# Performance work log

Hardware: AMD Instinct MI355X
Metric: run time of the kernel (lower is better)

The kernel has to match this reference:

```python
import jax, jax.numpy as jnp
import numpy as np

B, T, C, H = 8, 2048, 768, 64  # batch, seq_len, embedding_dim, head_size


def setup_inputs() -> dict:
    key = jax.random.key(0)
    k1, k2, k3, k4 = jax.random.split(key, 4)
    x = jax.random.normal(k1, (B, T, C), dtype=jnp.float32)
    attention_mask = jnp.ones((B, T), dtype=jnp.float32)
    # nn.Linear(C, H, bias=False) weights stored pre-transposed as (C, H)
    scale = 0.02
    Wq = jax.random.normal(k2, (C, H), dtype=jnp.float32) * scale
    Wk = jax.random.normal(k3, (C, H), dtype=jnp.float32) * scale
    Wv = jax.random.normal(k4, (C, H), dtype=jnp.float32) * scale
    return {"x": x, "attention_mask": attention_mask, "Wq": Wq, "Wk": Wk, "Wv": Wv}


def reference(x, attention_mask, Wq, Wk, Wv):
    # x: [B,T,C]; attention_mask: [B,T] (multiplied per query row)
    head_size = Wq.shape[-1]
    q = x @ Wq  # [B,T,H]
    k = x @ Wk  # [B,T,H]
    v = x @ Wv  # [B,T,H]
    inv_sqrt_h = jnp.asarray(1.0 / np.sqrt(head_size), x.dtype)
    s = jnp.einsum('bqh,bkh->bqk', q, k) * inv_sqrt_h  # [B,T,T]
    # attention_mask.unsqueeze(2) * qK ; masked_fill(qK == 0, -inf)
    s = attention_mask[:, :, None] * s
    s = jnp.where(s == 0, -jnp.inf, s)
    # causal tril mask
    seq = x.shape[1]
    tril = jnp.tril(jnp.ones((seq, seq), dtype=bool))
    s = jnp.where(tril[None, :, :], s, -jnp.inf)
    p = jax.nn.softmax(s, axis=-1)
    # dropout p=0.0 -> identity; nan cleanup (fully-masked rows)
    p = jnp.where(jnp.isnan(p), jnp.asarray(0.0, p.dtype), p)
    out = jnp.einsum('bqk,bkh->bqh', p, v)  # [B,T,H]
    return out
```

## Files before the change

### kernel.cpp

```cpp
#include <hip/hip_runtime.h>
#include <hip/hip_bf16.h>

#define B_ 8
#define T_ 2048
#define C_ 768
#define H_ 64
#define BT_ (B_*T_)

typedef __attribute__((ext_vector_type(8))) short bf16x8;
typedef __attribute__((ext_vector_type(4))) float f32x4;

__device__ __forceinline__ unsigned short f2bf(float x) {
    __hip_bfloat16 h = __float2bfloat16(x);
    return __builtin_bit_cast(unsigned short, h);
}

__device__ __forceinline__ bf16x8 cvt8(float4 a, float4 b) {
    bf16x8 r;
    r[0] = (short)f2bf(a.x); r[1] = (short)f2bf(a.y);
    r[2] = (short)f2bf(a.z); r[3] = (short)f2bf(a.w);
    r[4] = (short)f2bf(b.x); r[5] = (short)f2bf(b.y);
    r[6] = (short)f2bf(b.z); r[7] = (short)f2bf(b.w);
    return r;
}

__global__ __launch_bounds__(256) void wprep(
    const float* __restrict__ Wq, const float* __restrict__ Wk,
    const float* __restrict__ Wv, unsigned short* __restrict__ WTf)
{
    const int gc = blockIdx.x;
    const int t  = threadIdx.x;
    const int lane = t >> 2;
    const int j0   = (t & 3) * 2;
    const int q16  = lane & 15, quad = lane >> 4;
    const int k    = gc * 32 + quad * 8 + j0;
    #pragma unroll
    for (int f = 0; f < 12; f++) {
        const int row = f * 16 + q16;
        const int m = row >> 6, n = row & 63;
        const float* __restrict__ W = (m == 0) ? Wq : (m == 1) ? Wk : Wv;
        ushort2 u;
        u.x = f2bf(W[(size_t)k * H_ + n]);
        u.y = f2bf(W[(size_t)(k + 1) * H_ + n]);
        *(ushort2*)(WTf + (((size_t)gc * 12 + f) * 64 + lane) * 8 + j0) = u;
    }
}

__global__ __launch_bounds__(256, 4) void qkv_kernel(
    const float* __restrict__ x, const unsigned short* __restrict__ WTf,
    unsigned short* __restrict__ qF, unsigned short* __restrict__ kF,
    unsigned short* __restrict__ vF)
{
    __shared__ float mrg[3][64][49];
    const int tid  = threadIdx.x;
    const int w    = tid >> 6;
    const int lane = tid & 63;
    const int q16  = lane & 15, quad = lane >> 4;
    const int rowBase = blockIdx.x << 4;
    const int row  = rowBase + q16;

    const float* __restrict__ xp = x + (size_t)row * C_ + w * 192 + quad * 8;

    f32x4 acc[12] = {};
    #pragma unroll
    for (int c = 0; c < 6; c++) {
        const int gc = w * 6 + c;
        const unsigned short* __restrict__ wpc = WTf + ((size_t)gc * 12) * 512 + lane * 8;
        float4 xa = *(const float4*)(xp + c * 32);
        float4 xb = *(const float4*)(xp + c * 32 + 4);
        bf16x8 wf[12];
        #pragma unroll
        for (int f = 0; f < 12; f++)
            wf[f] = *(const bf16x8*)(wpc + f * 512);
        bf16x8 xf = cvt8(xa, xb);
        #pragma unroll
        for (int f = 0; f < 12; f++)
            acc[f] = __builtin_amdgcn_mfma_f32_16x16x32_bf16(wf[f], xf, acc[f], 0, 0, 0);
    }

    if (w > 0) {
        #pragma unroll
        for (int f = 0; f < 12; f++)
            #pragma unroll
            for (int r = 0; r < 4; r++) mrg[w - 1][lane][f * 4 + r] = acc[f][r];
    }
    __syncthreads();
    if (w == 0) {
        #pragma unroll
        for (int j = 0; j < 3; j++)
            #pragma unroll
            for (int f = 0; f < 12; f++)
                #pragma unroll
                for (int r = 0; r < 4; r++) acc[f][r] += mrg[j][lane][f * 4 + r];

        const size_t gt = (size_t)(rowBase >> 4);
        #pragma unroll
        for (int f = 0; f < 8; f++) {
            ushort4 u;
            u.x = f2bf(acc[f][0]); u.y = f2bf(acc[f][1]);
            u.z = f2bf(acc[f][2]); u.w = f2bf(acc[f][3]);
            const int n4 = f & 3;
            const int qp = (2 * n4 + (quad >> 1)) & 3;
            const int j0 = (quad & 1) * 4;
            unsigned short* __restrict__ dst = (f < 4) ? qF : kF;
            *(ushort4*)(dst + ((gt * 2 + (n4 >> 1)) * 64 + q16 + 16 * qp) * 8 + j0) = u;
        }
        const size_t g32 = (size_t)(rowBase >> 5);
        const int qv = ((rowBase >> 4) & 1) * 2 + (q16 >> 3);
        const int jv = q16 & 7;
        #pragma unroll
        for (int f = 8; f < 12; f++)
            #pragma unroll
            for (int r = 0; r < 4; r++)
                vF[((g32 * 4 + (f - 8)) * 64 + quad * 4 + r + 16 * qv) * 8 + jv] =
                    f2bf(acc[f][r]);
    }
}

__global__ __launch_bounds__(256) void attn_kernel(
    const unsigned short* __restrict__ qF, const unsigned short* __restrict__ kF,
    const unsigned short* __restrict__ vF, const float* __restrict__ mask,
    float* __restrict__ out)
{
    __shared__ __align__(16) unsigned short pS[4][16][88];
    __shared__ float oS[3][64][17];
    __shared__ float mlS[3][64][2];

    const int tid  = threadIdx.x;
    const int w    = tid >> 6;
    const int lane = tid & 63;
    const int q16  = lane & 15;
    const int quad = lane >> 4;
    const int bid  = blockIdx.x;
    const int b    = bid & 7;
    const int qt   = 127 - (bid >> 3);
    const int qrow = (qt << 4) + q16;

    const size_t qbase = ((size_t)(b * 128 + qt) * 2) * 512 + lane * 8;
    bf16x8 qf0 = *(const bf16x8*)(qF + qbase);
    bf16x8 qf1 = *(const bf16x8*)(qF + qbase + 512);
    const float maskv = mask[b * T_ + qrow] * 0.125f * 1.44269504f;

    f32x4 o[4] = {};
    float m_run = -__builtin_inff();
    float l_run = 0.f;

    const int niter = ((qt << 4) + 16 + 63) >> 6;
    for (int kt = w; kt < niter; kt += 4) {
        const int kbase = kt << 6;

        bf16x8 kf[8], vf[8];
        #pragma unroll
        for (int sub = 0; sub < 4; sub++) {
            const unsigned short* kp = kF + ((size_t)(b * 128 + kt * 4 + sub) * 2) * 512 + lane * 8;
            kf[2 * sub]     = *(const bf16x8*)(kp);
            kf[2 * sub + 1] = *(const bf16x8*)(kp + 512);
        }
        #pragma unroll
        for (int ht = 0; ht < 4; ht++) {
            const unsigned short* vp = vF + ((size_t)(b * 64 + kt * 2) * 4 + ht) * 512 + lane * 8;
            vf[2 * ht]     = *(const bf16x8*)(vp);
            vf[2 * ht + 1] = *(const bf16x8*)(vp + 4 * 512);
        }

        f32x4 sa[4] = {};
        #pragma unroll
        for (int sub = 0; sub < 4; sub++) {
            sa[sub] = __builtin_amdgcn_mfma_f32_16x16x32_bf16(kf[2 * sub],     qf0, sa[sub], 0, 0, 0);
            sa[sub] = __builtin_amdgcn_mfma_f32_16x16x32_bf16(kf[2 * sub + 1], qf1, sa[sub], 0, 0, 0);
        }

        float s[16];
        #pragma unroll
        for (int sub = 0; sub < 4; sub++)
            #pragma unroll
            for (int r = 0; r < 4; r++) {
                int kidx = kbase + sub * 16 + quad * 4 + r;
                float sv = sa[sub][r] * maskv;
                sv = (sv == 0.f) ? -__builtin_inff() : sv;
                sv = (kidx > qrow) ? -__builtin_inff() : sv;
                s[sub * 4 + r] = sv;
            }

        float mx = s[0];
        #pragma unroll
        for (int i2 = 1; i2 < 16; i2++) mx = fmaxf(mx, s[i2]);
        mx = fmaxf(mx, __shfl_xor(mx, 16));
        mx = fmaxf(mx, __shfl_xor(mx, 32));
        float m_new = fmaxf(m_run, mx);
        float m_use = (m_new == -__builtin_inff()) ? 0.f : m_new;
        float alpha = exp2f(m_run - m_use);
        float p[16], psum = 0.f;
        #pragma unroll
        for (int i2 = 0; i2 < 16; i2++) { p[i2] = exp2f(s[i2] - m_use); psum += p[i2]; }
        psum += __shfl_xor(psum, 16);
        psum += __shfl_xor(psum, 32);
        l_run = l_run * alpha + psum;
        m_run = m_new;
        #pragma unroll
        for (int ht = 0; ht < 4; ht++)
            #pragma unroll
            for (int r = 0; r < 4; r++) o[ht][r] *= alpha;

        #pragma unroll
        for (int sub = 0; sub < 4; sub++) {
            unsigned int lo = (unsigned int)f2bf(p[sub * 4 + 0]) | ((unsigned int)f2bf(p[sub * 4 + 1]) << 16);
            unsigned int hi = (unsigned int)f2bf(p[sub * 4 + 2]) | ((unsigned int)f2bf(p[sub * 4 + 3]) << 16);
            *(uint2*)&pS[w][q16][sub * 16 + quad * 4] = make_uint2(lo, hi);
        }
        bf16x8 pf0 = *(const bf16x8*)&pS[w][q16][quad * 8];
        bf16x8 pf1 = *(const bf16x8*)&pS[w][q16][32 + quad * 8];

        #pragma unroll
        for (int ht = 0; ht < 4; ht++) {
            o[ht] = __builtin_amdgcn_mfma_f32_16x16x32_bf16(vf[2 * ht],     pf0, o[ht], 0, 0, 0);
            o[ht] = __builtin_amdgcn_mfma_f32_16x16x32_bf16(vf[2 * ht + 1], pf1, o[ht], 0, 0, 0);
        }
    }

    if (w > 0) {
        mlS[w - 1][lane][0] = m_run;
        mlS[w - 1][lane][1] = l_run;
        #pragma unroll
        for (int ht = 0; ht < 4; ht++)
            #pragma unroll
            for (int r = 0; r < 4; r++) oS[w - 1][lane][ht * 4 + r] = o[ht][r];
    }
    __syncthreads();
    if (w == 0) {
        float mm[3], ll[3];
        float m = m_run;
        #pragma unroll
        for (int j = 0; j < 3; j++) {
            mm[j] = mlS[j][lane][0]; ll[j] = mlS[j][lane][1];
            m = fmaxf(m, mm[j]);
        }
        float mu = (m == -__builtin_inff()) ? 0.f : m;
        float a0 = exp2f(m_run - mu);
        float aj[3];
        float l = l_run * a0;
        #pragma unroll
        for (int j = 0; j < 3; j++) { aj[j] = exp2f(mm[j] - mu); l += ll[j] * aj[j]; }
        float invl = (l > 0.f) ? (1.f / l) : 0.f;
        #pragma unroll
        for (int ht = 0; ht < 4; ht++) {
            float4 ov;
            float vx = o[ht][0] * a0, vy = o[ht][1] * a0, vz = o[ht][2] * a0, vw2 = o[ht][3] * a0;
            #pragma unroll
            for (int j = 0; j < 3; j++) {
                vx += oS[j][lane][ht * 4 + 0] * aj[j];
                vy += oS[j][lane][ht * 4 + 1] * aj[j];
                vz += oS[j][lane][ht * 4 + 2] * aj[j];
                vw2 += oS[j][lane][ht * 4 + 3] * aj[j];
            }
            ov.x = vx * invl; ov.y = vy * invl; ov.z = vz * invl; ov.w = vw2 * invl;
            *(float4*)(out + ((size_t)(b * T_) + qrow) * H_ + ht * 16 + quad * 4) = ov;
        }
    }
}

extern "C" void kernel_launch(void* const* d_in, const int* in_sizes, int n_in,
                              void* d_out, int out_size, void* d_ws, size_t ws_size,
                              hipStream_t stream) {
    const float* x    = (const float*)d_in[0];
    const float* mask = (const float*)d_in[1];
    const float* Wq   = (const float*)d_in[2];
    const float* Wk   = (const float*)d_in[3];
    const float* Wv   = (const float*)d_in[4];
    float* out = (float*)d_out;

    unsigned short* qf = (unsigned short*)d_ws;
    unsigned short* kf = qf + (size_t)BT_ * H_;
    unsigned short* vf = kf + (size_t)BT_ * H_;
    unsigned short* wt = vf + (size_t)BT_ * H_;

    wprep<<<24, 256, 0, stream>>>(Wq, Wk, Wv, wt);
    qkv_kernel<<<BT_ / 16, 256, 0, stream>>>(x, wt, qf, kf, vf);
    attn_kernel<<<B_ * (T_ / 16), 256, 0, stream>>>(qf, kf, vf, mask, out);
}
```

Before: 122.7 us.

## Process 32 rows per QKV block to reuse weight fragments; coalesce weight prep via LDS

The QKV projection kernel now handles two 16-row tiles per block, so each loaded bf16 weight fragment feeds two MFMAs. This halves the weight traffic per row and the number of blocks. The weight-prep kernel is rewritten to read rows coalesced into a shared tile and transpose them there, and it is spread over 72 blocks instead of 24. The cost is more accumulator registers, reflected in lowering the occupancy hint to 2, plus an extra LDS merge phase with added barriers.

```diff
diff --git a/kernel.cpp b/kernel.cpp
--- a/kernel.cpp
+++ b/kernel.cpp
@@ -28,25 +28,37 @@
     const float* __restrict__ Wq, const float* __restrict__ Wk,
     const float* __restrict__ Wv, unsigned short* __restrict__ WTf)
 {
-    const int gc = blockIdx.x;
-    const int t  = threadIdx.x;
-    const int lane = t >> 2;
-    const int j0   = (t & 3) * 2;
-    const int q16  = lane & 15, quad = lane >> 4;
-    const int k    = gc * 32 + quad * 8 + j0;
-    #pragma unroll
-    for (int f = 0; f < 12; f++) {
-        const int row = f * 16 + q16;
-        const int m = row >> 6, n = row & 63;
-        const float* __restrict__ W = (m == 0) ? Wq : (m == 1) ? Wk : Wv;
-        ushort2 u;
-        u.x = f2bf(W[(size_t)k * H_ + n]);
-        u.y = f2bf(W[(size_t)(k + 1) * H_ + n]);
-        *(ushort2*)(WTf + (((size_t)gc * 12 + f) * 64 + lane) * 8 + j0) = u;
-    }
-}
-
-__global__ __launch_bounds__(256, 4) void qkv_kernel(
+    __shared__ float tile[32][68];
+    const int bid = blockIdx.x;
+    const int m = bid / 24, gc = bid % 24;
+    const float* __restrict__ W = (m == 0) ? Wq : (m == 1) ? Wk : Wv;
+    const int t = threadIdx.x;
+    {
+        const int r = t >> 3, c0 = (t & 7) * 8;
+        float4 a = *(const float4*)(W + (size_t)(gc * 32 + r) * H_ + c0);
+        float4 b = *(const float4*)(W + (size_t)(gc * 32 + r) * H_ + c0 + 4);
+        *(float4*)&tile[r][c0]     = a;
+        *(float4*)&tile[r][c0 + 4] = b;
+    }
+    __syncthreads();
+    const int fl = t >> 6, lane = t & 63;
+    const int q16 = lane & 15, quad = lane >> 4;
+    const int f = m * 4 + fl;
+    ushort4 u0, u1;
+    u0.x = f2bf(tile[quad * 8 + 0][fl * 16 + q16]);
+    u0.y = f2bf(tile[quad * 8 + 1][fl * 16 + q16]);
+    u0.z = f2bf(tile[quad * 8 + 2][fl * 16 + q16]);
+    u0.w = f2bf(tile[quad * 8 + 3][fl * 16 + q16]);
+    u1.x = f2bf(tile[quad * 8 + 4][fl * 16 + q16]);
+    u1.y = f2bf(tile[quad * 8 + 5][fl * 16 + q16]);
+    u1.z = f2bf(tile[quad * 8 + 6][fl * 16 + q16]);
+    u1.w = f2bf(tile[quad * 8 + 7][fl * 16 + q16]);
+    unsigned short* __restrict__ dst = WTf + ((size_t)(gc * 12 + f) * 64 + lane) * 8;
+    *(ushort4*)(dst)     = u0;
+    *(ushort4*)(dst + 4) = u1;
+}
+
+__global__ __launch_bounds__(256, 2) void qkv_kernel(
     const float* __restrict__ x, const unsigned short* __restrict__ WTf,
     unsigned short* __restrict__ qF, unsigned short* __restrict__ kF,
     unsigned short* __restrict__ vF)
@@ -56,44 +68,35 @@
     const int w    = tid >> 6;
     const int lane = tid & 63;
     const int q16  = lane & 15, quad = lane >> 4;
-    const int rowBase = blockIdx.x << 4;
-    const int row  = rowBase + q16;
-
-    const float* __restrict__ xp = x + (size_t)row * C_ + w * 192 + quad * 8;
-
-    f32x4 acc[12] = {};
+    const int rowBase = blockIdx.x << 5;
+
+    const float* __restrict__ xp0 = x + (size_t)(rowBase + q16) * C_ + w * 192 + quad * 8;
+    const float* __restrict__ xp1 = xp0 + (size_t)16 * C_;
+
+    f32x4 acc0[12] = {}, acc1[12] = {};
     #pragma unroll
     for (int c = 0; c < 6; c++) {
         const int gc = w * 6 + c;
         const unsigned short* __restrict__ wpc = WTf + ((size_t)gc * 12) * 512 + lane * 8;
-        float4 xa = *(const float4*)(xp + c * 32);
-        float4 xb = *(const float4*)(xp + c * 32 + 4);
+        float4 xa0 = *(const float4*)(xp0 + c * 32);
+        float4 xb0 = *(const float4*)(xp0 + c * 32 + 4);
+        float4 xa1 = *(const float4*)(xp1 + c * 32);
+        float4 xb1 = *(const float4*)(xp1 + c * 32 + 4);
         bf16x8 wf[12];
         #pragma unroll
         for (int f = 0; f < 12; f++)
             wf[f] = *(const bf16x8*)(wpc + f * 512);
-        bf16x8 xf = cvt8(xa, xb);
-        #pragma unroll
-        for (int f = 0; f < 12; f++)
-            acc[f] = __builtin_amdgcn_mfma_f32_16x16x32_bf16(wf[f], xf, acc[f], 0, 0, 0);
-    }
-
-    if (w > 0) {
-        #pragma unroll
-        for (int f = 0; f < 12; f++)
-            #pragma unroll
-            for (int r = 0; r < 4; r++) mrg[w - 1][lane][f * 4 + r] = acc[f][r];
-    }
-    __syncthreads();
-    if (w == 0) {
-        #pragma unroll
-        for (int j = 0; j < 3; j++)
-            #pragma unroll
-            for (int f = 0; f < 12; f++)
-                #pragma unroll
-                for (int r = 0; r < 4; r++) acc[f][r] += mrg[j][lane][f * 4 + r];
-
-        const size_t gt = (size_t)(rowBase >> 4);
+        bf16x8 xf0 = cvt8(xa0, xb0);
+        bf16x8 xf1 = cvt8(xa1, xb1);
+        #pragma unroll
+        for (int f = 0; f < 12; f++) {
+            acc0[f] = __builtin_amdgcn_mfma_f32_16x16x32_bf16(wf[f], xf0, acc0[f], 0, 0, 0);
+            acc1[f] = __builtin_amdgcn_mfma_f32_16x16x32_bf16(wf[f], xf1, acc1[f], 0, 0, 0);
+        }
+    }
+
+    auto flush = [&](f32x4* acc, int gtile) {
+        const size_t gt = (size_t)gtile;
         #pragma unroll
         for (int f = 0; f < 8; f++) {
             ushort4 u;
@@ -105,8 +108,8 @@
             unsigned short* __restrict__ dst = (f < 4) ? qF : kF;
             *(ushort4*)(dst + ((gt * 2 + (n4 >> 1)) * 64 + q16 + 16 * qp) * 8 + j0) = u;
         }
-        const size_t g32 = (size_t)(rowBase >> 5);
-        const int qv = ((rowBase >> 4) & 1) * 2 + (q16 >> 3);
+        const size_t g32 = (size_t)(gtile >> 1);
+        const int qv = (gtile & 1) * 2 + (q16 >> 3);
         const int jv = q16 & 7;
         #pragma unroll
         for (int f = 8; f < 12; f++)
@@ -114,6 +117,40 @@
             for (int r = 0; r < 4; r++)
                 vF[((g32 * 4 + (f - 8)) * 64 + quad * 4 + r + 16 * qv) * 8 + jv] =
                     f2bf(acc[f][r]);
+    };
+
+    if (w > 0) {
+        #pragma unroll
+        for (int f = 0; f < 12; f++)
+            #pragma unroll
+            for (int r = 0; r < 4; r++) mrg[w - 1][lane][f * 4 + r] = acc0[f][r];
+    }
+    __syncthreads();
+    if (w == 0) {
+        #pragma unroll
+        for (int j = 0; j < 3; j++)
+            #pragma unroll
+            for (int f = 0; f < 12; f++)
+                #pragma unroll
+                for (int r = 0; r < 4; r++) acc0[f][r] += mrg[j][lane][f * 4 + r];
+        flush(acc0, rowBase >> 4);
+    }
+    __syncthreads();
+    if (w > 0) {
+        #pragma unroll
+        for (int f = 0; f < 12; f++)
+            #pragma unroll
+            for (int r = 0; r < 4; r++) mrg[w - 1][lane][f * 4 + r] = acc1[f][r];
+    }
+    __syncthreads();
+    if (w == 0) {
+        #pragma unroll
+        for (int j = 0; j < 3; j++)
+            #pragma unroll
+            for (int f = 0; f < 12; f++)
+                #pragma unroll
+                for (int r = 0; r < 4; r++) acc1[f][r] += mrg[j][lane][f * 4 + r];
+        flush(acc1, (rowBase >> 4) + 1);
     }
 }
 
@@ -274,7 +311,7 @@
     unsigned short* vf = kf + (size_t)BT_ * H_;
     unsigned short* wt = vf + (size_t)BT_ * H_;
 
-    wprep<<<24, 256, 0, stream>>>(Wq, Wk, Wv, wt);
-    qkv_kernel<<<BT_ / 16, 256, 0, stream>>>(x, wt, qf, kf, vf);
+    wprep<<<72, 256, 0, stream>>>(Wq, Wk, Wv, wt);
+    qkv_kernel<<<BT_ / 32, 256, 0, stream>>>(x, wt, qf, kf, vf);
     attn_kernel<<<B_ * (T_ / 16), 256, 0, stream>>>(qf, kf, vf, mask, out);
 }
```

Result: faster. 120.3 us (-2.0%).
